# Kernel tuning notes

Measured on AMD Instinct MI355X. Metric: run time of the kernel, lower is better.

## Reference

```python
import jax, jax.numpy as jnp
import numpy as np

S, B, C = 1024, 2, 20
COORD, NOOBJ, NPRED = 5.0, 0.5, 5


def setup_inputs() -> dict:
    key = jax.random.key(0)
    k1, k2, k3 = jax.random.split(key, 3)
    pred = jax.random.normal(k1, (S, S, B * NPRED + C), dtype=jnp.float32)
    # target: box part uniform in [0,1) (w,h must be >=0 for sqrt), classes one-hot
    box_t = jax.random.uniform(k2, (S, S, B * NPRED), dtype=jnp.float32)
    cls_idx = jax.random.randint(k3, (S, S), 0, C)
    cls_t = jax.nn.one_hot(cls_idx, C, dtype=jnp.float32)
    target = jnp.concatenate([box_t, cls_t], axis=-1)
    return {"pred": pred, "target": target}


def reference(pred, target):
    # boxes: [S, S, B, 5] with (conf, x, y, w, h)
    boxes_p = pred[..., : B * NPRED].reshape(S, S, B, NPRED)
    boxes_t = target[..., : B * NPRED].reshape(S, S, B, NPRED)

    conf_p, x_p, y_p = boxes_p[..., 0], boxes_p[..., 1], boxes_p[..., 2]
    w_p = jnp.sqrt(jnp.abs(boxes_p[..., 3]))
    h_p = jnp.sqrt(jnp.abs(boxes_p[..., 4]))

    conf_t, x_t, y_t = boxes_t[..., 0], boxes_t[..., 1], boxes_t[..., 2]
    w_t = jnp.sqrt(boxes_t[..., 3])
    h_t = jnp.sqrt(boxes_t[..., 4])

    xy_loss = jnp.sum((jnp.square(x_t - x_p) + jnp.square(y_t - y_p)) * conf_t)
    box_loss = jnp.sum((jnp.square(w_t - w_p) + jnp.square(h_t - h_p)) * conf_t)
    conf_sq = jnp.square(conf_t - conf_p)
    confidence_loss = jnp.sum(conf_sq * conf_t)
    noobj_confidence_loss = jnp.sum(conf_sq * (1.0 - conf_t))

    # class loss: only cells whose target class vector sums to exactly 1.0
    pred_cls = pred[..., B * NPRED :].reshape(S * S, C)
    tgt_cls = target[..., B * NPRED :].reshape(S * S, C)
    cell_mask = (jnp.sum(tgt_cls, axis=-1) == 1.0).astype(pred.dtype)  # [S*S]
    per_cell = jnp.sum(jnp.square(tgt_cls) - jnp.square(pred_cls), axis=-1)
    cls_loss = jnp.sum(per_cell * cell_mask)

    return COORD * xy_loss + COORD * box_loss + confidence_loss + noobj_confidence_loss + cls_loss
```

## Files before the change

### kernel.cpp

```cpp
#include <hip/hip_runtime.h>


constexpr int S_DIM       = 1024;
constexpr int NCELL       = S_DIM * S_DIM;
constexpr int CH          = 30;
constexpr int BLOCK       = 256;
constexpr int TILE_CELLS  = 256;
constexpr int TILE_FLOATS = TILE_CELLS * CH;
constexpr int TILE_F4     = TILE_FLOATS / 4;
constexpr int NTILES      = NCELL / TILE_CELLS;
constexpr int GRID        = 2048;

__device__ __forceinline__ float wave_reduce_sum(float v) {
#pragma unroll
    for (int off = 32; off > 0; off >>= 1)
        v += __shfl_down(v, off, 64);
    return v;
}

__global__ __launch_bounds__(BLOCK, 2) void yolo_partial_kernel(
        const float* __restrict__ pred,
        const float* __restrict__ tgt,
        float* __restrict__ partial) {
    __shared__ float sp[TILE_FLOATS];
    __shared__ float st[TILE_FLOATS];

    const int tid = threadIdx.x;
    float acc = 0.0f;

    for (int tile = blockIdx.x; tile < NTILES; tile += GRID) {
        const float4* gp = reinterpret_cast<const float4*>(pred) + (size_t)tile * TILE_F4;
        const float4* gt = reinterpret_cast<const float4*>(tgt)  + (size_t)tile * TILE_F4;
        float4* s4p = reinterpret_cast<float4*>(sp);
        float4* s4t = reinterpret_cast<float4*>(st);

        __syncthreads();
#pragma unroll
        for (int j = 0; j < 7; ++j) {
            const int idx = j * BLOCK + tid;
            s4p[idx] = gp[idx];
            s4t[idx] = gt[idx];
        }
        {
            const int idx = 7 * BLOCK + tid;
            if (idx < TILE_F4) { s4p[idx] = gp[idx]; s4t[idx] = gt[idx]; }
        }
        __syncthreads();

        const float* pp = sp + tid * CH;
        const float* tt = st + tid * CH;

#pragma unroll
        for (int b = 0; b < 2; ++b) {
            const float conf_p = pp[5 * b + 0];
            const float x_p    = pp[5 * b + 1];
            const float y_p    = pp[5 * b + 2];
            const float w_p    = sqrtf(fabsf(pp[5 * b + 3]));
            const float h_p    = sqrtf(fabsf(pp[5 * b + 4]));
            const float conf_t = tt[5 * b + 0];
            const float x_t    = tt[5 * b + 1];
            const float y_t    = tt[5 * b + 2];
            const float w_t    = sqrtf(tt[5 * b + 3]);
            const float h_t    = sqrtf(tt[5 * b + 4]);

            const float dx = x_t - x_p, dy = y_t - y_p;
            const float dw = w_t - w_p, dh = h_t - h_p;
            const float dc = conf_t - conf_p;

            acc += 5.0f * ((dx * dx + dy * dy) * conf_t)
                 + 5.0f * ((dw * dw + dh * dh) * conf_t)
                 + dc * dc;
        }

        float ssum = 0.0f, per_cell = 0.0f;
#pragma unroll
        for (int k = 0; k < 20; ++k) {
            const float tc = tt[10 + k];
            const float pc = pp[10 + k];
            ssum     += tc;
            per_cell += tc * tc - pc * pc;
        }
        acc += (ssum == 1.0f) ? per_cell : 0.0f;
    }

    __shared__ float red[BLOCK / 64];
    const int lane = tid & 63;
    const int wid  = tid >> 6;

    float v = wave_reduce_sum(acc);
    if (lane == 0) red[wid] = v;
    __syncthreads();
    if (wid == 0) {
        v = (lane < (BLOCK / 64)) ? red[lane] : 0.0f;
        v = wave_reduce_sum(v);
        if (lane == 0) partial[blockIdx.x] = v;
    }
}

__global__ __launch_bounds__(256) void yolo_final_kernel(
        const float* __restrict__ partial,
        float* __restrict__ out,
        int n) {
    float acc = 0.0f;
    for (int i = threadIdx.x; i < n; i += 256)
        acc += partial[i];

    __shared__ float red[4];
    const int lane = threadIdx.x & 63;
    const int wid  = threadIdx.x >> 6;
    float v = wave_reduce_sum(acc);
    if (lane == 0) red[wid] = v;
    __syncthreads();
    if (wid == 0) {
        v = (lane < 4) ? red[lane] : 0.0f;
        v = wave_reduce_sum(v);
        if (lane == 0) out[0] = v;
    }
}

extern "C" void kernel_launch(void* const* d_in, const int* in_sizes, int n_in,
                              void* d_out, int out_size, void* d_ws, size_t ws_size,
                              hipStream_t stream) {
    const float* pred = (const float*)d_in[0];
    const float* tgt  = (const float*)d_in[1];
    float* out        = (float*)d_out;
    float* partial    = (float*)d_ws;

    yolo_partial_kernel<<<GRID, BLOCK, 0, stream>>>(pred, tgt, partial);
    yolo_final_kernel<<<1, 256, 0, stream>>>(partial, out, GRID);
}
```

Before: 46.83 us.

## Split each cell across two threads with smaller tiles for higher occupancy

Tiles shrink from 256 to 128 cells, which halves the LDS used per block, and the launch bound rises to five blocks per CU. Each cell is now handled by a pair of threads. One thread takes one of the two boxes and half of the class channels, and the two halves of the class sum are combined with a lane shuffle before the one-hot mask test. The aim is more resident waves to hide global-load latency in this bandwidth-bound reduction. The cost is more tile iterations per block and an extra shuffle.

New measurement: 45.21 us. 3.5% less time.

```diff
diff --git a/kernel.cpp b/kernel.cpp
--- a/kernel.cpp
+++ b/kernel.cpp
@@ -5,7 +5,7 @@
 constexpr int NCELL       = S_DIM * S_DIM;
 constexpr int CH          = 30;
 constexpr int BLOCK       = 256;
-constexpr int TILE_CELLS  = 256;
+constexpr int TILE_CELLS  = 128;
 constexpr int TILE_FLOATS = TILE_CELLS * CH;
 constexpr int TILE_F4     = TILE_FLOATS / 4;
 constexpr int NTILES      = NCELL / TILE_CELLS;
@@ -18,14 +18,16 @@
     return v;
 }
 
-__global__ __launch_bounds__(BLOCK, 2) void yolo_partial_kernel(
+__global__ __launch_bounds__(BLOCK, 5) void yolo_partial_kernel(
         const float* __restrict__ pred,
         const float* __restrict__ tgt,
         float* __restrict__ partial) {
     __shared__ float sp[TILE_FLOATS];
     __shared__ float st[TILE_FLOATS];
 
-    const int tid = threadIdx.x;
+    const int tid  = threadIdx.x;
+    const int cell = tid >> 1;
+    const int half = tid & 1;
     float acc = 0.0f;
 
     for (int tile = blockIdx.x; tile < NTILES; tile += GRID) {
@@ -36,32 +38,32 @@
 
         __syncthreads();
 #pragma unroll
-        for (int j = 0; j < 7; ++j) {
+        for (int j = 0; j < 3; ++j) {
             const int idx = j * BLOCK + tid;
             s4p[idx] = gp[idx];
             s4t[idx] = gt[idx];
         }
         {
-            const int idx = 7 * BLOCK + tid;
+            const int idx = 3 * BLOCK + tid;
             if (idx < TILE_F4) { s4p[idx] = gp[idx]; s4t[idx] = gt[idx]; }
         }
         __syncthreads();
 
-        const float* pp = sp + tid * CH;
-        const float* tt = st + tid * CH;
+        const float* pp = sp + cell * CH;
+        const float* tt = st + cell * CH;
 
-#pragma unroll
-        for (int b = 0; b < 2; ++b) {
-            const float conf_p = pp[5 * b + 0];
-            const float x_p    = pp[5 * b + 1];
-            const float y_p    = pp[5 * b + 2];
-            const float w_p    = sqrtf(fabsf(pp[5 * b + 3]));
-            const float h_p    = sqrtf(fabsf(pp[5 * b + 4]));
-            const float conf_t = tt[5 * b + 0];
-            const float x_t    = tt[5 * b + 1];
-            const float y_t    = tt[5 * b + 2];
-            const float w_t    = sqrtf(tt[5 * b + 3]);
-            const float h_t    = sqrtf(tt[5 * b + 4]);
+        {
+            const int o = 5 * half;
+            const float conf_p = pp[o + 0];
+            const float x_p    = pp[o + 1];
+            const float y_p    = pp[o + 2];
+            const float w_p    = sqrtf(fabsf(pp[o + 3]));
+            const float h_p    = sqrtf(fabsf(pp[o + 4]));
+            const float conf_t = tt[o + 0];
+            const float x_t    = tt[o + 1];
+            const float y_t    = tt[o + 2];
+            const float w_t    = sqrtf(tt[o + 3]);
+            const float h_t    = sqrtf(tt[o + 4]);
 
             const float dx = x_t - x_p, dy = y_t - y_p;
             const float dw = w_t - w_p, dh = h_t - h_p;
@@ -73,14 +75,16 @@
         }
 
         float ssum = 0.0f, per_cell = 0.0f;
+        const int co = 10 + 10 * half;
 #pragma unroll
-        for (int k = 0; k < 20; ++k) {
-            const float tc = tt[10 + k];
-            const float pc = pp[10 + k];
+        for (int k = 0; k < 10; ++k) {
+            const float tc = tt[co + k];
+            const float pc = pp[co + k];
             ssum     += tc;
             per_cell += tc * tc - pc * pc;
         }
-        acc += (ssum == 1.0f) ? per_cell : 0.0f;
+        const float tot = ssum + __shfl_xor(ssum, 1, 64);
+        acc += (tot == 1.0f) ? per_cell : 0.0f;
     }
 
     __shared__ float red[BLOCK / 64];
```
